# Performance work log

Measured on AMD Instinct MI355X. Metric: run time of the kernel, lower is better.

Reference implementation:

```python
import jax, jax.numpy as jnp
import numpy as np

B, S, D = 2, 2048, 1024
H, HD = 16, 64
INIT = 0.02

def setup_inputs() -> dict:
    key = jax.random.key(0)
    k1, k2, k3 = jax.random.split(key, 3)
    x = jax.random.normal(k1, (B, S, D), dtype=jnp.float32)
    w_attn = jax.random.normal(k2, (D, 3 * D), dtype=jnp.float32) * INIT
    b_attn = jnp.zeros((3 * D,), dtype=jnp.float32)
    w_proj = jax.random.normal(k3, (D, D), dtype=jnp.float32) * INIT
    b_proj = jnp.zeros((D,), dtype=jnp.float32)
    return {"x": x, "w_attn": w_attn, "b_attn": b_attn, "w_proj": w_proj, "b_proj": b_proj}

def reference(x, w_attn, b_attn, w_proj, b_proj):
    # c_attn: [B,S,D] -> [B,S,3D]
    hidden = jnp.einsum('bse,ef->bsf', x, w_attn) + b_attn
    q, k, v = jnp.split(hidden, 3, axis=-1)
    # split heads -> [B,S,H,HD]
    q = q.reshape(B, S, H, HD) / jnp.sqrt(jnp.float32(HD))
    k = k.reshape(B, S, H, HD)
    v = v.reshape(B, S, H, HD)
    # scores: [B,H,S,S]
    scores = jnp.einsum('bqhd,bkhd->bhqk', q, k)
    causal = jnp.tril(jnp.ones((S, S), dtype=bool))  # [S,S]
    big_neg = jnp.finfo(jnp.float32).min
    scores = jnp.where(causal[None, None, :, :], scores, big_neg)
    weights = jax.nn.softmax(scores, axis=-1)
    z = jnp.einsum('bhqk,bkhd->bqhd', weights, v)
    merged = z.reshape(B, S, D)
    out = jnp.einsum('bse,ef->bsf', merged, w_proj) + b_proj
    return out
```

## Files before the change

### kernel.cpp

```cpp
#include <hip/hip_runtime.h>
#include <hip/hip_bf16.h>

typedef __attribute__((ext_vector_type(8))) short bf16x8;
typedef __attribute__((ext_vector_type(4))) float f32x4;
typedef unsigned short u16;
typedef unsigned int u32;

#define B_ 2
#define S_ 2048
#define D_ 1024
#define H_ 16
#define HD_ 64

#define LOG2E 1.44269504088896340736f

__device__ __forceinline__ u16 f2bf(float f) {
    __hip_bfloat16 h = __float2bfloat16(f);
    u16 r;
    __builtin_memcpy(&r, &h, 2);
    return r;
}

__device__ __forceinline__ float ex2(float x) {
    float r;
    asm("v_exp_f32 %0, %1" : "=v"(r) : "v"(x));
    return r;
}

__device__ __forceinline__ void gload16(const u16* gsrc, u16* lds_base) {
    __builtin_amdgcn_global_load_lds(
        (const __attribute__((address_space(1))) void*)gsrc,
        (__attribute__((address_space(3))) void*)lds_base, 16, 0, 0);
}

__global__ __launch_bounds__(256) void prep(
    const float* __restrict__ x, u16* __restrict__ x_bf,
    const float* __restrict__ wa, u16* __restrict__ waT,
    const float* __restrict__ wp, u16* __restrict__ wpT) {
    __shared__ float t[32][33];
    const int bid = blockIdx.x;
    const int tid = threadIdx.x;
    if (bid < 4096) {
        int i = bid * 256 + tid;
        float4 v = ((const float4*)x)[i];
        ushort4 o;
        o.x = f2bf(v.x); o.y = f2bf(v.y); o.z = f2bf(v.z); o.w = f2bf(v.w);
        ((ushort4*)x_bf)[i] = o;
        return;
    }
    const float* in;
    u16* out;
    int R = 1024, C, bx, by;
    if (bid < 4096 + 3072) {
        in = wa; out = waT; C = 3072;
        int idx = bid - 4096;
        bx = idx % 96; by = idx / 96;
    } else {
        in = wp; out = wpT; C = 1024;
        int idx = bid - 7168;
        bx = idx % 32; by = idx / 32;
    }
    const int c0 = bx * 32, r0 = by * 32;
    const int lx = tid & 31, ly = tid >> 5;
#pragma unroll
    for (int i = 0; i < 4; ++i)
        t[ly + i * 8][lx] = in[(size_t)(r0 + ly + i * 8) * C + c0 + lx];
    __syncthreads();
#pragma unroll
    for (int i = 0; i < 4; ++i)
        out[(size_t)(c0 + ly + i * 8) * R + r0 + lx] = f2bf(t[lx][ly + i * 8]);
}

__global__ __launch_bounds__(512, 1) void gemm192(
    const u16* __restrict__ A, const u16* __restrict__ Bt,
    const float* __restrict__ bias,
    u16* __restrict__ oQ, u16* __restrict__ oK, u16* __restrict__ oV) {
    extern __shared__ u16 lds[];
    u16* Al[2] = {lds, lds + 16384};
    u16* Bl[2] = {lds + 32768, lds + 32768 + 12288};

    const int tid = threadIdx.x;
    const int lane = tid & 63, w = tid >> 6;
    const int wm = w >> 2, wn = w & 3;
    const int l15 = lane & 15, lg = lane >> 4;
    const int lin = blockIdx.y * 16 + blockIdx.x;
    const int nl = (lin & 7) * 32 + (lin >> 3);
    const int m0 = (nl >> 4) * 256, n0 = (nl & 15) * 192;

    const int lrow = lane >> 3;
    const int csrc = ((lane & 7) * 8) ^ ((lrow & 7) * 8);
    const u16* pA = A + (size_t)(m0 + w * 32 + lrow) * 1024 + csrc;
    const u16* pB = Bt + (size_t)(n0 + w * 24 + lrow) * 1024 + csrc;

    const int sw8 = (l15 & 7) * 8;
    const int c0 = (lg * 8) ^ sw8;
    const int c1 = (32 + lg * 8) ^ sw8;
    const int abase = (wm * 128 + l15) * 64;
    const int bbase = (wn * 48 + l15) * 64;

    f32x4 acc[8][3] = {};
    bf16x8 afr[4][2], bfr[3][2];

#define STGA(bb, tt) { \
    _Pragma("unroll") for (int i_ = 0; i_ < 4; ++i_) \
        gload16(pA + (size_t)(tt) * 64 + i_ * 8192, Al[bb] + w * 2048 + i_ * 512); }
#define STGB(bb, tt) { \
    _Pragma("unroll") for (int j_ = 0; j_ < 3; ++j_) \
        gload16(pB + (size_t)(tt) * 64 + j_ * 8192, Bl[bb] + w * 1536 + j_ * 512); }

#define RDA(bb, AH) \
    _Pragma("unroll") for (int mt_ = 0; mt_ < 4; ++mt_) { \
        afr[mt_][0] = *(const bf16x8*)&Al[bb][abase + (AH) * 4096 + mt_ * 1024 + c0]; \
        afr[mt_][1] = *(const bf16x8*)&Al[bb][abase + (AH) * 4096 + mt_ * 1024 + c1]; }

#define RDB(bb) \
    _Pragma("unroll") for (int nt_ = 0; nt_ < 3; ++nt_) { \
        bfr[nt_][0] = *(const bf16x8*)&Bl[bb][bbase + nt_ * 1024 + c0]; \
        bfr[nt_][1] = *(const bf16x8*)&Bl[bb][bbase + nt_ * 1024 + c1]; }

#define MFMA24(AH) \
    __builtin_amdgcn_s_setprio(1); \
    _Pragma("unroll") for (int mt_ = 0; mt_ < 4; ++mt_) \
    _Pragma("unroll") for (int nt_ = 0; nt_ < 3; ++nt_) { \
        acc[(AH)*4+mt_][nt_] = __builtin_amdgcn_mfma_f32_16x16x32_bf16( \
            afr[mt_][0], bfr[nt_][0], acc[(AH)*4+mt_][nt_], 0, 0, 0); \
        acc[(AH)*4+mt_][nt_] = __builtin_amdgcn_mfma_f32_16x16x32_bf16( \
            afr[mt_][1], bfr[nt_][1], acc[(AH)*4+mt_][nt_], 0, 0, 0); } \
    __builtin_amdgcn_s_setprio(0);

#define BAR __builtin_amdgcn_s_barrier();
#define VMC3 { asm volatile("s_waitcnt vmcnt(3)" ::: "memory"); __builtin_amdgcn_sched_barrier(0); }
#define VMC0 { asm volatile("s_waitcnt vmcnt(0)" ::: "memory"); __builtin_amdgcn_sched_barrier(0); }

    STGB(0, 0); STGA(0, 0); STGB(1, 1);
    VMC3; BAR;

#pragma unroll 1
    for (int t = 0; t < 8; ++t) {
        const bool nf = (t < 7);
        RDA(0, 0) RDB(0)
        STGA(1, 2 * t + 1);
        BAR; MFMA24(0) BAR;
        RDA(0, 1)
        if (nf) STGB(0, 2 * t + 2);
        BAR; MFMA24(1)
        if (nf) { VMC3 } else { VMC0 }
        BAR;
        RDA(1, 0) RDB(1)
        if (nf) STGA(0, 2 * t + 2);
        BAR; MFMA24(0) BAR;
        RDA(1, 1)
        if (nf) STGB(1, 2 * t + 3);
        BAR; MFMA24(1)
        if (nf) { VMC3 }
        BAR;
    }

#pragma unroll
    for (int mt = 0; mt < 8; ++mt) {
#pragma unroll
        for (int nt = 0; nt < 3; ++nt) {
            const int n_g = n0 + wn * 48 + nt * 16 + l15;
            const int m_b = m0 + wm * 128 + mt * 16 + lg * 4;
            const float bs = bias[n_g];
            const int which = n_g >> 10;
            const int nn = n_g & 1023;
            const int h = nn >> 6, hd = nn & 63;
            const int bb = m_b >> 11, s = m_b & 2047;
            if (which == 2) {
                ushort4 pv;
                pv.x = f2bf(acc[mt][nt][0] + bs);
                pv.y = f2bf(acc[mt][nt][1] + bs);
                pv.z = f2bf(acc[mt][nt][2] + bs);
                pv.w = f2bf(acc[mt][nt][3] + bs);
                *(ushort4*)&oV[((size_t)(bb * H_ + h) * HD_ + hd) * S_ + s] = pv;
            } else {
                u16* dst = which == 0 ? oQ : oK;
                const float scale = which == 0 ? (0.125f * LOG2E) : 1.0f;
#pragma unroll
                for (int r = 0; r < 4; ++r)
                    dst[((size_t)(bb * H_ + h) * S_ + s + r) * HD_ + hd] =
                        f2bf((acc[mt][nt][r] + bs) * scale);
            }
        }
    }
#undef STGA
#undef STGB
#undef RDA
#undef RDB
#undef MFMA24
#undef BAR
#undef VMC3
#undef VMC0
}

__global__ __launch_bounds__(512, 1) void gemm_proj(
    const u16* __restrict__ A, const u16* __restrict__ Bt,
    const float* __restrict__ bias, float* __restrict__ oF) {
    extern __shared__ u16 lds[];
    u16* Al[2] = {lds, lds + 8192};
    u16* Bl[2] = {lds + 16384, lds + 16384 + 8192};

    const int tid = threadIdx.x;
    const int lane = tid & 63, w = tid >> 6;
    const int wm = w >> 2, wn = w & 3;
    const int l15 = lane & 15, lg = lane >> 4;
    const int lin = blockIdx.y * 8 + blockIdx.x;
    const int nl = (lin & 7) * 32 + (lin >> 3);
    const int m0 = (nl >> 3) * 128, n0 = (nl & 7) * 128;

    const int lrow = lane >> 3;
    const int csrc = ((lane & 7) * 8) ^ ((lrow & 7) * 8);
    const u16* pA = A + (size_t)(m0 + w * 16 + lrow) * 1024 + csrc;
    const u16* pB = Bt + (size_t)(n0 + w * 16 + lrow) * 1024 + csrc;

    const int sw8 = (l15 & 7) * 8;
    const int c0 = (lg * 8) ^ sw8;
    const int c1 = (32 + lg * 8) ^ sw8;
    const int abase = (wm * 64 + l15) * 64;
    const int bbase = (wn * 32 + l15) * 64;

    f32x4 acc[4][2] = {};
    bf16x8 afr[4], bfr[2][2];

#define PSTGA(bb, tt) { \
    _Pragma("unroll") for (int i_ = 0; i_ < 2; ++i_) \
        gload16(pA + (size_t)(tt) * 64 + i_ * 8192, Al[bb] + w * 1024 + i_ * 512); }
#define PSTGB(bb, tt) { \
    _Pragma("unroll") for (int i_ = 0; i_ < 2; ++i_) \
        gload16(pB + (size_t)(tt) * 64 + i_ * 8192, Bl[bb] + w * 1024 + i_ * 512); }

#define PRDA(bb, G) \
    _Pragma("unroll") for (int mt_ = 0; mt_ < 4; ++mt_) \
        afr[mt_] = *(const bf16x8*)&Al[bb][abase + mt_ * 1024 + ((G) ? c1 : c0)];

#define PRDB(bb) \
    _Pragma("unroll") for (int nt_ = 0; nt_ < 2; ++nt_) { \
        bfr[nt_][0] = *(const bf16x8*)&Bl[bb][bbase + nt_ * 1024 + c0]; \
        bfr[nt_][1] = *(const bf16x8*)&Bl[bb][bbase + nt_ * 1024 + c1]; }

#define PMFMA8(G) \
    __builtin_amdgcn_s_setprio(1); \
    _Pragma("unroll") for (int mt_ = 0; mt_ < 4; ++mt_) \
    _Pragma("unroll") for (int nt_ = 0; nt_ < 2; ++nt_) \
        acc[mt_][nt_] = __builtin_amdgcn_mfma_f32_16x16x32_bf16( \
            afr[mt_], bfr[nt_][G], acc[mt_][nt_], 0, 0, 0); \
    __builtin_amdgcn_s_setprio(0);

#define BAR __builtin_amdgcn_s_barrier();
#define VMC2 { asm volatile("s_waitcnt vmcnt(2)" ::: "memory"); __builtin_amdgcn_sched_barrier(0); }
#define VMC0 { asm volatile("s_waitcnt vmcnt(0)" ::: "memory"); __builtin_amdgcn_sched_barrier(0); }

    PSTGB(0, 0); PSTGA(0, 0); PSTGB(1, 1);
    VMC2; BAR;

#pragma unroll 1
    for (int t = 0; t < 8; ++t) {
        const bool nf = (t < 7);
        PRDA(0, 0) PRDB(0)
        PSTGA(1, 2 * t + 1);
        BAR; PMFMA8(0) BAR;
        PRDA(0, 1)
        if (nf) PSTGB(0, 2 * t + 2);
        BAR; PMFMA8(1)
        if (nf) { VMC2 } else { VMC0 }
        BAR;
        PRDA(1, 0) PRDB(1)
        if (nf) PSTGA(0, 2 * t + 2);
        BAR; PMFMA8(0) BAR;
        PRDA(1, 1)
        if (nf) PSTGB(1, 2 * t + 3);
        BAR; PMFMA8(1)
        if (nf) { VMC2 }
        BAR;
    }

#pragma unroll
    for (int mt = 0; mt < 4; ++mt)
#pragma unroll
        for (int nt = 0; nt < 2; ++nt) {
            const int n_g = n0 + wn * 32 + nt * 16 + l15;
            const int m_b = m0 + wm * 64 + mt * 16 + lg * 4;
            const float bs = bias[n_g];
#pragma unroll
            for (int r = 0; r < 4; ++r)
                oF[(size_t)(m_b + r) * 1024 + n_g] = acc[mt][nt][r] + bs;
        }
#undef PSTGA
#undef PSTGB
#undef PRDA
#undef PRDB
#undef PMFMA8
#undef BAR
#undef VMC2
#undef VMC0
}

__global__ __launch_bounds__(256, 2) void attn9(
    const u16* __restrict__ Q, const u16* __restrict__ Kp,
    const u16* __restrict__ VT, u16* __restrict__ Om) {
    extern __shared__ u16 lds[];
    u16* Kl = lds;
    u16* Vl = lds + 16384;
    u16* Pl = lds + 32768;
    const int tid = threadIdx.x;
    const int lane = tid & 63, w = tid >> 6;
    const int l15 = lane & 15, lg = lane >> 4;
    const int hw = blockIdx.x;
    const int bid = (hw & 7) * 64 + (hw >> 3);
    const int bh = bid >> 4, p = bid & 15;
    const int b = bh >> 4, h = bh & 15;
    const size_t baseK = (size_t)bh * (S_ * HD_);
    const u16* gk = Kp + baseK;
    const u16* gv = VT + (size_t)bh * (HD_ * S_);

    const int lrow = lane >> 3;
    const int csK = ((lane & 7) * 8) ^ ((lrow & 7) * 8);
    const int lg2 = lane >> 4;
    const int csV0 = ((lane & 15) * 8) ^ (lg2 * 8);
    const int csV1 = ((lane & 15) * 8) ^ ((4 + lg2) * 8);
    const u16* gkp[4];
    const u16* gvp[4];
#pragma unroll
    for (int i = 0; i < 4; ++i) {
        gkp[i] = gk + (size_t)(w * 32 + i * 8 + lrow) * HD_ + csK;
        gvp[i] = gv + (size_t)(w * 16 + i * 4 + lg2) * S_ + ((i & 1) ? csV1 : csV0);
    }
    u16* ldsK = Kl + w * 2048;
    u16* ldsV = Vl + w * 2048;

    const int sw = (l15 & 7) * 8;
    const int roK0 = l15 * 128 + 2 * ((lg * 8) ^ sw);
    const int roK1 = l15 * 128 + 2 * ((32 + lg * 8) ^ sw);
    int po[4];
#pragma unroll
    for (int g = 0; g < 4; ++g) po[g] = 2 * ((g * 32 + lg * 8) ^ sw);
    const char* kbase = (const char*)Kl;
    const char* vbase = (const char*)Vl;
    char* plw = (char*)(Pl + w * 2048);
    const int prb = l15 * 256;
    int pwo[8];
#pragma unroll
    for (int nt = 0; nt < 8; ++nt) pwo[nt] = prb + 2 * ((nt * 16 + lg * 4) ^ sw);

    const int qbA = 31 - p, qbB = p;
    const int kitA = (qbA + 2) >> 1, kitB = (qbB + 2) >> 1;
    const int qgA = qbA * 64 + w * 16 + l15;
    const int qgB = qbB * 64 + w * 16 + l15;

    const bf16x8 qa0 = *(const bf16x8*)&Q[baseK + (size_t)qgA * HD_ + lg * 8];
    const bf16x8 qa1 = *(const bf16x8*)&Q[baseK + (size_t)qgA * HD_ + 32 + lg * 8];
    const bf16x8 qb0 = *(const bf16x8*)&Q[baseK + (size_t)qgB * HD_ + lg * 8];
    const bf16x8 qb1 = *(const bf16x8*)&Q[baseK + (size_t)qgB * HD_ + 32 + lg * 8];

    f32x4 accA[4] = {}, accB[4] = {};
    float lA = 0.0f, lB = 0.0f;

#pragma unroll
    for (int i = 0; i < 4; ++i) {
        gload16(gkp[i], ldsK + i * 512);
        gload16(gvp[i], ldsV + i * 512);
    }

#define QK8(sc, q0v, q1v) { \
    _Pragma("unroll") for (int nt_ = 0; nt_ < 8; ++nt_) { \
        bf16x8 kf = *(const bf16x8*)(kb + nt_ * 2048 + roK0); \
        sc[nt_] = __builtin_amdgcn_mfma_f32_16x16x32_bf16(kf, q0v, f32x4{}, 0, 0, 0); } \
    _Pragma("unroll") for (int nt_ = 0; nt_ < 8; ++nt_) { \
        bf16x8 kf = *(const bf16x8*)(kb + nt_ * 2048 + roK1); \
        sc[nt_] = __builtin_amdgcn_mfma_f32_16x16x32_bf16(kf, q1v, sc[nt_], 0, 0, 0); } }

#define SMFIX(sc, lrun) { \
    float ps_ = 0.0f; \
    _Pragma("unroll") for (int nt_ = 0; nt_ < 8; ++nt_) { \
        float a_ = ex2(sc[nt_][0]); \
        float c_ = ex2(sc[nt_][1]); \
        float d_ = ex2(sc[nt_][2]); \
        float e_ = ex2(sc[nt_][3]); \
        sc[nt_][0] = a_; sc[nt_][1] = c_; sc[nt_][2] = d_; sc[nt_][3] = e_; \
        ps_ += (a_ + c_) + (d_ + e_); } \
    lrun += ps_; }

#define PWR(sc) { \
    _Pragma("unroll") for (int nt_ = 0; nt_ < 8; ++nt_) { \
        ushort4 pk_; \
        pk_.x = f2bf(sc[nt_][0]); pk_.y = f2bf(sc[nt_][1]); \
        pk_.z = f2bf(sc[nt_][2]); pk_.w = f2bf(sc[nt_][3]); \
        *(ushort4*)(plw + pwo[nt_]) = pk_; } }

#define PV8(accv) { \
    _Pragma("unroll") for (int g_ = 0; g_ < 4; ++g_) { \
        bf16x8 pb_ = *(const bf16x8*)(plw + prb + po[g_]); \
        _Pragma("unroll") for (int dt_ = 0; dt_ < 4; ++dt_) { \
            bf16x8 vf_ = *(const bf16x8*)(vb + (dt_ * 16 + l15) * 256 + po[g_]); \
            accv[dt_] = __builtin_amdgcn_mfma_f32_16x16x32_bf16(vf_, pb_, accv[dt_], 0, 0, 0); } } }

#define MASK8(sc, tc) { \
    _Pragma("unroll") for (int nt_ = 0; nt_ < 8; ++nt_) \
    _Pragma("unroll") for (int r_ = 0; r_ < 4; ++r_) \
        if (nt_ * 16 + lg * 4 + r_ > (tc)) sc[nt_][r_] = -1e30f; }

    for (int it = 0; it < kitA; ++it) {
        const int cur = it & 1;
        const int bo = cur * 16384;
        __syncthreads();
        if (it + 1 < kitA) {
            const int be = (cur ^ 1) * 8192;
            const int kt2 = (it + 1) * 128;
#pragma unroll
            for (int i = 0; i < 4; ++i) {
                gload16(gkp[i] + kt2 * HD_, ldsK + be + i * 512);
                gload16(gvp[i] + kt2, ldsV + be + i * 512);
            }
        }
        const char* kb = kbase + bo;
        const char* vb = vbase + bo;
        const bool doB = (it < kitB);

        f32x4 scA[8], scB[8];
        __builtin_amdgcn_s_setprio(1);
        QK8(scA, qa0, qa1)
        if (doB) QK8(scB, qb0, qb1)
        __builtin_amdgcn_s_setprio(0);
        if (it == kitA - 1) MASK8(scA, qgA - it * 128)
        if (doB && it == kitB - 1) MASK8(scB, qgB - it * 128)
        SMFIX(scA, lA)
        PWR(scA)
        if (doB) SMFIX(scB, lB)
        __builtin_amdgcn_s_setprio(1);
        PV8(accA)
        __builtin_amdgcn_s_setprio(0);
        if (doB) {
            PWR(scB)
            __builtin_amdgcn_s_setprio(1);
            PV8(accB)
            __builtin_amdgcn_s_setprio(0);
        }
    }
#undef QK8
#undef SMFIX
#undef PWR
#undef PV8
#undef MASK8

    {
        float lt = lA + __shfl_xor(lA, 16, 64);
        lt = lt + __shfl_xor(lt, 32, 64);
        const float rl = 1.0f / lt;
#pragma unroll
        for (int dt = 0; dt < 4; ++dt) {
            ushort4 ov;
            ov.x = f2bf(accA[dt][0] * rl);
            ov.y = f2bf(accA[dt][1] * rl);
            ov.z = f2bf(accA[dt][2] * rl);
            ov.w = f2bf(accA[dt][3] * rl);
            *(ushort4*)&Om[((size_t)b * S_ + qgA) * D_ + h * HD_ + dt * 16 + lg * 4] = ov;
        }
    }
    {
        float lt = lB + __shfl_xor(lB, 16, 64);
        lt = lt + __shfl_xor(lt, 32, 64);
        const float rl = 1.0f / lt;
#pragma unroll
        for (int dt = 0; dt < 4; ++dt) {
            ushort4 ov;
            ov.x = f2bf(accB[dt][0] * rl);
            ov.y = f2bf(accB[dt][1] * rl);
            ov.z = f2bf(accB[dt][2] * rl);
            ov.w = f2bf(accB[dt][3] * rl);
            *(ushort4*)&Om[((size_t)b * S_ + qgB) * D_ + h * HD_ + dt * 16 + lg * 4] = ov;
        }
    }
}

extern "C" void kernel_launch(void* const* d_in, const int* in_sizes, int n_in,
                              void* d_out, int out_size, void* d_ws, size_t ws_size,
                              hipStream_t stream) {
    const float* x      = (const float*)d_in[0];
    const float* w_attn = (const float*)d_in[1];
    const float* b_attn = (const float*)d_in[2];
    const float* w_proj = (const float*)d_in[3];
    const float* b_proj = (const float*)d_in[4];
    float* out = (float*)d_out;

    char* ws = (char*)d_ws;
    const size_t XE = (size_t)B_ * S_ * D_;
    u16* x_bf = (u16*)ws;            ws += XE * 2;
    u16* waT  = (u16*)ws;            ws += (size_t)3 * D_ * D_ * 2;
    u16* wpT  = (u16*)ws;            ws += (size_t)D_ * D_ * 2;
    u16* Qb   = (u16*)ws;            ws += XE * 2;
    u16* Kb   = (u16*)ws;            ws += XE * 2;
    u16* Vt   = (u16*)ws;            ws += XE * 2;
    u16* Mg   = x_bf;

    hipFuncSetAttribute((const void*)gemm192,
                        hipFuncAttributeMaxDynamicSharedMemorySize, 114688);
    hipFuncSetAttribute((const void*)attn9,
                        hipFuncAttributeMaxDynamicSharedMemorySize, 81920);
    hipFuncSetAttribute((const void*)gemm_proj,
                        hipFuncAttributeMaxDynamicSharedMemorySize, 65536);

    prep<<<8192, 256, 0, stream>>>(x, x_bf, w_attn, waT, w_proj, wpT);

    gemm192<<<dim3(16, 16), 512, 114688, stream>>>(x_bf, waT, b_attn, Qb, Kb, Vt);

    attn9<<<B_ * H_ * 16, 256, 81920, stream>>>(Qb, Kb, Vt, Mg);

    gemm_proj<<<dim3(8, 32), 512, 65536, stream>>>(Mg, wpT, b_proj, out);
}
```

Before: 90.71 us.

## Keep softmax probabilities in registers and permute V layout for PV MFMA

The attention kernel no longer writes the bf16 probability tile to LDS and reads it back. Instead it packs the P values into registers with v_cvt_pk_bf16_f32 and feeds them straight into 16x16x16 bf16 MFMAs. To make this work, the QKV GEMM epilogue writes V^T with a permuted sequence order so each lane's V fragment lines up with its register-held P columns. This removes the P LDS round trip and cuts the LDS allocation from 80KB to 64KB, at the cost of twice as many smaller MFMA instructions in the PV step.

Result: slower. 93.83 us (+3.4%).

```diff
diff --git a/kernel.cpp b/kernel.cpp
--- a/kernel.cpp
+++ b/kernel.cpp
@@ -2,6 +2,7 @@
 #include <hip/hip_bf16.h>
 
 typedef __attribute__((ext_vector_type(8))) short bf16x8;
+typedef __attribute__((ext_vector_type(4))) short bf16x4;
 typedef __attribute__((ext_vector_type(4))) float f32x4;
 typedef unsigned short u16;
 typedef unsigned int u32;
@@ -31,6 +32,17 @@
     __builtin_amdgcn_global_load_lds(
         (const __attribute__((address_space(1))) void*)gsrc,
         (__attribute__((address_space(3))) void*)lds_base, 16, 0, 0);
+}
+
+__device__ __forceinline__ f32x4 mfma16(bf16x4 a, bf16x4 b, f32x4 c) {
+#if __has_builtin(__builtin_amdgcn_mfma_f32_16x16x16_bf16)
+    return __builtin_amdgcn_mfma_f32_16x16x16_bf16(a, b, c, 0, 0, 0);
+#elif __has_builtin(__builtin_amdgcn_mfma_f32_16x16x16bf16_1k)
+    return __builtin_amdgcn_mfma_f32_16x16x16bf16_1k(a, b, c, 0, 0, 0);
+#else
+    asm("v_mfma_f32_16x16x16_bf16 %0, %1, %2, %0" : "+v"(c) : "v"(a), "v"(b));
+    return c;
+#endif
 }
 
 __global__ __launch_bounds__(256) void prep(
@@ -173,7 +185,9 @@
                 pv.y = f2bf(acc[mt][nt][1] + bs);
                 pv.z = f2bf(acc[mt][nt][2] + bs);
                 pv.w = f2bf(acc[mt][nt][3] + bs);
-                *(ushort4*)&oV[((size_t)(bb * H_ + h) * HD_ + hd) * S_ + s] = pv;
+                const int ws = s & 127, blk = s >> 7;
+                const int sp = blk * 128 + ((ws >> 2) & 3) * 32 + ((ws >> 4) << 2);
+                *(ushort4*)&oV[((size_t)(bb * H_ + h) * HD_ + hd) * S_ + sp] = pv;
             } else {
                 u16* dst = which == 0 ? oQ : oK;
                 const float scale = which == 0 ? (0.125f * LOG2E) : 1.0f;
@@ -296,13 +310,12 @@
 #undef VMC0
 }
 
-__global__ __launch_bounds__(256, 2) void attn9(
+__global__ __launch_bounds__(256, 2) void attn10(
     const u16* __restrict__ Q, const u16* __restrict__ Kp,
     const u16* __restrict__ VT, u16* __restrict__ Om) {
     extern __shared__ u16 lds[];
     u16* Kl = lds;
     u16* Vl = lds + 16384;
-    u16* Pl = lds + 32768;
     const int tid = threadIdx.x;
     const int lane = tid & 63, w = tid >> 6;
     const int l15 = lane & 15, lg = lane >> 4;
@@ -332,16 +345,11 @@
     const int sw = (l15 & 7) * 8;
     const int roK0 = l15 * 128 + 2 * ((lg * 8) ^ sw);
     const int roK1 = l15 * 128 + 2 * ((32 + lg * 8) ^ sw);
-    int po[4];
-#pragma unroll
-    for (int g = 0; g < 4; ++g) po[g] = 2 * ((g * 32 + lg * 8) ^ sw);
+    int pvo[4];
+#pragma unroll
+    for (int g2 = 0; g2 < 4; ++g2) pvo[g2] = 2 * ((lg * 32 + g2 * 8) ^ sw);
     const char* kbase = (const char*)Kl;
     const char* vbase = (const char*)Vl;
-    char* plw = (char*)(Pl + w * 2048);
-    const int prb = l15 * 256;
-    int pwo[8];
-#pragma unroll
-    for (int nt = 0; nt < 8; ++nt) pwo[nt] = prb + 2 * ((nt * 16 + lg * 4) ^ sw);
 
     const int qbA = 31 - p, qbB = p;
     const int kitA = (qbA + 2) >> 1, kitB = (qbB + 2) >> 1;
@@ -381,19 +389,22 @@
         ps_ += (a_ + c_) + (d_ + e_); } \
     lrun += ps_; }
 
-#define PWR(sc) { \
+#define PACK8(sc, pw) { \
     _Pragma("unroll") for (int nt_ = 0; nt_ < 8; ++nt_) { \
-        ushort4 pk_; \
-        pk_.x = f2bf(sc[nt_][0]); pk_.y = f2bf(sc[nt_][1]); \
-        pk_.z = f2bf(sc[nt_][2]); pk_.w = f2bf(sc[nt_][3]); \
-        *(ushort4*)(plw + pwo[nt_]) = pk_; } }
-
-#define PV8(accv) { \
-    _Pragma("unroll") for (int g_ = 0; g_ < 4; ++g_) { \
-        bf16x8 pb_ = *(const bf16x8*)(plw + prb + po[g_]); \
-        _Pragma("unroll") for (int dt_ = 0; dt_ < 4; ++dt_) { \
-            bf16x8 vf_ = *(const bf16x8*)(vb + (dt_ * 16 + l15) * 256 + po[g_]); \
-            accv[dt_] = __builtin_amdgcn_mfma_f32_16x16x32_bf16(vf_, pb_, accv[dt_], 0, 0, 0); } } }
+        u32 w0_, w1_; \
+        asm("v_cvt_pk_bf16_f32 %0, %1, %2" : "=v"(w0_) : "v"(sc[nt_][0]), "v"(sc[nt_][1])); \
+        asm("v_cvt_pk_bf16_f32 %0, %1, %2" : "=v"(w1_) : "v"(sc[nt_][2]), "v"(sc[nt_][3])); \
+        u32 t_[2] = {w0_, w1_}; \
+        __builtin_memcpy(&pw[nt_], t_, 8); } }
+
+#define PV16(accv, pw) { \
+    _Pragma("unroll") for (int g2_ = 0; g2_ < 4; ++g2_) \
+    _Pragma("unroll") for (int dt_ = 0; dt_ < 4; ++dt_) { \
+        bf16x8 vf_ = *(const bf16x8*)(vb + (dt_ * 16 + l15) * 256 + pvo[g2_]); \
+        bf16x4 vlo_ = __builtin_shufflevector(vf_, vf_, 0, 1, 2, 3); \
+        bf16x4 vhi_ = __builtin_shufflevector(vf_, vf_, 4, 5, 6, 7); \
+        accv[dt_] = mfma16(vlo_, pw[2 * g2_], accv[dt_]); \
+        accv[dt_] = mfma16(vhi_, pw[2 * g2_ + 1], accv[dt_]); } }
 
 #define MASK8(sc, tc) { \
     _Pragma("unroll") for (int nt_ = 0; nt_ < 8; ++nt_) \
@@ -418,6 +429,7 @@
         const bool doB = (it < kitB);
 
         f32x4 scA[8], scB[8];
+        bf16x4 pwA[8], pwB[8];
         __builtin_amdgcn_s_setprio(1);
         QK8(scA, qa0, qa1)
         if (doB) QK8(scB, qb0, qb1)
@@ -425,22 +437,17 @@
         if (it == kitA - 1) MASK8(scA, qgA - it * 128)
         if (doB && it == kitB - 1) MASK8(scB, qgB - it * 128)
         SMFIX(scA, lA)
-        PWR(scA)
-        if (doB) SMFIX(scB, lB)
+        PACK8(scA, pwA)
+        if (doB) { SMFIX(scB, lB) PACK8(scB, pwB) }
         __builtin_amdgcn_s_setprio(1);
-        PV8(accA)
+        PV16(accA, pwA)
+        if (doB) PV16(accB, pwB)
         __builtin_amdgcn_s_setprio(0);
-        if (doB) {
-            PWR(scB)
-            __builtin_amdgcn_s_setprio(1);
-            PV8(accB)
-            __builtin_amdgcn_s_setprio(0);
-        }
     }
 #undef QK8
 #undef SMFIX
-#undef PWR
-#undef PV8
+#undef PACK8
+#undef PV16
 #undef MASK8
 
     {
@@ -495,8 +502,8 @@
 
     hipFuncSetAttribute((const void*)gemm192,
                         hipFuncAttributeMaxDynamicSharedMemorySize, 114688);
-    hipFuncSetAttribute((const void*)attn9,
-                        hipFuncAttributeMaxDynamicSharedMemorySize, 81920);
+    hipFuncSetAttribute((const void*)attn10,
+                        hipFuncAttributeMaxDynamicSharedMemorySize, 65536);
     hipFuncSetAttribute((const void*)gemm_proj,
                         hipFuncAttributeMaxDynamicSharedMemorySize, 65536);
 
@@ -504,7 +511,7 @@
 
     gemm192<<<dim3(16, 16), 512, 114688, stream>>>(x_bf, waT, b_attn, Qb, Kb, Vt);
 
-    attn9<<<B_ * H_ * 16, 256, 81920, stream>>>(Qb, Kb, Vt, Mg);
+    attn10<<<B_ * H_ * 16, 256, 65536, stream>>>(Qb, Kb, Vt, Mg);
 
     gemm_proj<<<dim3(8, 32), 512, 65536, stream>>>(Mg, wpT, b_proj, out);
 }
```
